# Optimization experiments

Hardware: AMD Instinct MI355X
Metric: run time of the kernel (lower is better)

The kernel has to match this reference:

```python
import jax, jax.numpy as jnp
import numpy as np

IDENTITY_WEIGHT = 0.5
EPS_NORM = 1e-6   # channel RMSNorm eps
EPS_COS = 1e-12   # cosine-sim norm eps (matches torch F.normalize default)


def setup_inputs() -> dict:
    key = jax.random.key(0)
    k1, k2 = jax.random.split(key)
    B, C, H, W = 32, 768, 32, 32
    X = jax.random.normal(k1, (B, C, H, W), dtype=jnp.float32)
    # 1x1 conv weight [out=3C, in=C] (kernel dims squeezed)
    W_in = jax.random.normal(k2, (3 * C, C), dtype=jnp.float32) * (C ** -0.5)
    return {"X": X, "W_in": W_in}


def _cos_sim(t):
    # normalize over the flattened spatial axis (last dim)
    return t / (jnp.linalg.norm(t, axis=-1, keepdims=True) + EPS_COS)


def reference(X, W_in):
    B, C, H, W = X.shape
    # norm: parameter-free RMS over channel dim
    Xn = X * jax.lax.rsqrt(jnp.mean(X * X, axis=1, keepdims=True) + EPS_NORM)
    # 1x1 conv (bias-free) == channel GEMM: [B,3C,H,W]
    qkv = jnp.einsum('oc,bchw->bohw', W_in, Xn)
    K = qkv[:, :C].reshape(B, 1, C, H * W)       # b h c (x y), h=1
    V = qkv[:, C:2 * C].reshape(B, 1, C, H * W)
    # cosine similarity per channel over spatial positions: [B,1,C,1]
    A = jnp.sum(_cos_sim(K) * _cos_sim(V), axis=-1, keepdims=True)
    # affine gate with identity weight (feature_map_attn = identity)
    A = (1.0 - IDENTITY_WEIGHT) * A + IDENTITY_WEIGHT
    A = A.reshape(B, C, 1, 1)  # 'b 1 c 1 -> b c 1 1'
    return A * X
```

## Files before the change

### kernel.cpp

```cpp
#include <hip/hip_runtime.h>
#include <hip/hip_bf16.h>
#include <cstdint>
#include <cstddef>


#define B_   32
#define C_   768
#define HW_  1024
#define CHW_ (C_ * HW_)
#define EPS_NORM 1e-6f
#define EPS_COS  1e-12f

using f32x4  = __attribute__((ext_vector_type(4))) float;
using bf16x8 = __attribute__((ext_vector_type(8))) short;

__device__ inline unsigned short f2bf(float f) {
    union { float f; unsigned u; } v; v.f = f;
    unsigned u = v.u;
    u += 0x7fffu + ((u >> 16) & 1u);
    return (unsigned short)(u >> 16);
}

__device__ __forceinline__ void load16_lds(const unsigned short* g, short* l) {
    __builtin_amdgcn_global_load_lds(
        (const __attribute__((address_space(1))) unsigned int*)g,
        (__attribute__((address_space(3))) unsigned int*)l,
        16, 0, 0);
}

__global__ void wconv_kernel(const float* __restrict__ W, unsigned short* __restrict__ Wbf) {
    const int i = blockIdx.x * 256 + threadIdx.x;
    const float4 v = reinterpret_cast<const float4*>(W)[i];
    ushort4 o;
    o.x = f2bf(v.x); o.y = f2bf(v.y); o.z = f2bf(v.z); o.w = f2bf(v.w);
    reinterpret_cast<ushort4*>(Wbf)[i] = o;
}

__global__ void sumsq_kernel(const float* __restrict__ X, float* __restrict__ ssum) {
    const int b  = blockIdx.y;
    const int c0 = blockIdx.x * 32;
    const int t  = threadIdx.x;
    const float4* xp = reinterpret_cast<const float4*>(X + (size_t)b * CHW_ + (size_t)c0 * HW_) + t;
    float4 s = {0.f, 0.f, 0.f, 0.f};
    #pragma unroll 8
    for (int c = 0; c < 32; ++c) {
        float4 v = xp[c * 256];
        s.x += v.x * v.x; s.y += v.y * v.y; s.z += v.z * v.z; s.w += v.w * v.w;
    }
    float* dst = ssum + b * HW_ + t * 4;
    atomicAdd(dst + 0, s.x);
    atomicAdd(dst + 1, s.y);
    atomicAdd(dst + 2, s.z);
    atomicAdd(dst + 3, s.w);
}

__global__ __launch_bounds__(256) void xnt_kernel(const float* __restrict__ X,
                                                  const float* __restrict__ ssum,
                                                  unsigned short* __restrict__ Xnt) {
    const int b   = blockIdx.z;
    const int c0  = blockIdx.y * 64;
    const int hw0 = blockIdx.x * 64;
    const int tid = threadIdx.x;
    __shared__ short T[64][78];

    #pragma unroll
    for (int it = 0; it < 4; ++it) {
        int q  = it * 256 + tid;
        int r  = q >> 4;
        int c4 = (q & 15) * 4;
        const float4 x = *reinterpret_cast<const float4*>(
            X + (size_t)b * CHW_ + (size_t)(c0 + r) * HW_ + hw0 + c4);
        const float4 s = *reinterpret_cast<const float4*>(ssum + b * HW_ + hw0 + c4);
        ushort4 o;
        o.x = f2bf(x.x * rsqrtf(s.x * (1.f / 768.f) + EPS_NORM));
        o.y = f2bf(x.y * rsqrtf(s.y * (1.f / 768.f) + EPS_NORM));
        o.z = f2bf(x.z * rsqrtf(s.z * (1.f / 768.f) + EPS_NORM));
        o.w = f2bf(x.w * rsqrtf(s.w * (1.f / 768.f) + EPS_NORM));
        *reinterpret_cast<ushort4*>(&T[r][c4]) = o;
    }
    __syncthreads();
    #pragma unroll
    for (int it = 0; it < 2; ++it) {
        int q  = it * 256 + tid;
        int rp = q >> 3;
        int cc = (q & 7) * 8;
        __align__(16) unsigned short tmp[8];
        #pragma unroll
        for (int j = 0; j < 8; ++j) tmp[j] = (unsigned short)T[cc + j][rp];
        *reinterpret_cast<uint4*>(
            Xnt + (size_t)b * CHW_ + (size_t)(hw0 + rp) * C_ + c0 + cc) =
            *reinterpret_cast<const uint4*>(tmp);
    }
}

__global__ __launch_bounds__(256, 2) void gemm_kernel(
        const unsigned short* __restrict__ Wbf,
        const unsigned short* __restrict__ Xnt,
        float* __restrict__ wsA) {
    const int n0   = blockIdx.x * 128;
    const int c0   = blockIdx.y * 128;
    const int b    = blockIdx.z;
    const int tid  = threadIdx.x;
    const int lane = tid & 63;
    const int wave = tid >> 6;
    const int wm   = (wave >> 1) * 64;
    const int wn   = (wave & 1) * 64;
    const int quad = lane >> 4;
    const int l15  = lane & 15;

    __shared__ short sAK[128][64];
    __shared__ short sAV[128][64];
    __shared__ short sB [128][64];

    const f32x4 zero = {0.f, 0.f, 0.f, 0.f};
    f32x4 accK[4][4], accV[4][4];
    #pragma unroll
    for (int i = 0; i < 4; ++i)
        #pragma unroll
        for (int j = 0; j < 4; ++j) { accK[i][j] = zero; accV[i][j] = zero; }

    const size_t wk_base = (size_t)c0 * 768;
    const size_t wv_base = (size_t)(768 + c0) * 768;
    const size_t xb      = (size_t)b * CHW_ + (size_t)n0 * 768;

    size_t goff[4];
    int    lrow[4];
    #pragma unroll
    for (int it = 0; it < 4; ++it) {
        int q   = it * 256 + tid;
        int row = q >> 3;
        int gch = (q & 7) ^ (row & 7);
        goff[it] = (size_t)row * 768 + gch * 8;
        lrow[it] = row & ~7;
    }

    for (int k0 = 0; k0 < 768; k0 += 64) {
        __syncthreads();
        #pragma unroll
        for (int it = 0; it < 4; ++it) {
            load16_lds(Wbf + wk_base + goff[it] + k0, &sAK[lrow[it]][0]);
            load16_lds(Wbf + wv_base + goff[it] + k0, &sAV[lrow[it]][0]);
            load16_lds(Xnt + xb      + goff[it] + k0, &sB [lrow[it]][0]);
        }
        __syncthreads();

        #pragma unroll
        for (int kh = 0; kh < 2; ++kh) {
            bf16x8 aK[4], aV[4], bF[4];
            #pragma unroll
            for (int i = 0; i < 4; ++i) {
                const int rA = wm + 16 * i + l15;
                const int sA = ((kh * 4 + quad) ^ (rA & 7)) * 8;
                aK[i] = *reinterpret_cast<const bf16x8*>(&sAK[rA][sA]);
                aV[i] = *reinterpret_cast<const bf16x8*>(&sAV[rA][sA]);
                const int rB = wn + 16 * i + l15;
                const int sBo = ((kh * 4 + quad) ^ (rB & 7)) * 8;
                bF[i] = *reinterpret_cast<const bf16x8*>(&sB[rB][sBo]);
            }
            #pragma unroll
            for (int i = 0; i < 4; ++i)
                #pragma unroll
                for (int j = 0; j < 4; ++j) {
                    accK[i][j] = __builtin_amdgcn_mfma_f32_16x16x32_bf16(aK[i], bF[j], accK[i][j], 0, 0, 0);
                    accV[i][j] = __builtin_amdgcn_mfma_f32_16x16x32_bf16(aV[i], bF[j], accV[i][j], 0, 0, 0);
                }
        }
    }

    #pragma unroll
    for (int i = 0; i < 4; ++i) {
        #pragma unroll
        for (int r = 0; r < 4; ++r) {
            float pd = 0.f, pk = 0.f, pv = 0.f;
            #pragma unroll
            for (int j = 0; j < 4; ++j) {
                float kk = accK[i][j][r], vv = accV[i][j][r];
                pd += kk * vv; pk += kk * kk; pv += vv * vv;
            }
            #pragma unroll
            for (int off = 1; off < 16; off <<= 1) {
                pd += __shfl_xor(pd, off);
                pk += __shfl_xor(pk, off);
                pv += __shfl_xor(pv, off);
            }
            if (l15 == 0) {
                int c = c0 + wm + 16 * i + 4 * quad + r;
                float* dst = wsA + ((size_t)b * C_ + c) * 3;
                atomicAdd(dst + 0, pd);
                atomicAdd(dst + 1, pk);
                atomicAdd(dst + 2, pv);
            }
        }
    }
}

__global__ void final_kernel(const float* __restrict__ X, const float* __restrict__ wsA,
                             float* __restrict__ out) {
    const int bc = blockIdx.x;
    const float* a = wsA + (size_t)bc * 3;
    const float pd = a[0], pk = a[1], pv = a[2];
    const float A = pd / ((sqrtf(pk) + EPS_COS) * (sqrtf(pv) + EPS_COS));
    const float g = 0.5f * A + 0.5f;
    const size_t i4 = (size_t)bc * 256 + threadIdx.x;
    float4 x = reinterpret_cast<const float4*>(X)[i4];
    float4 o;
    o.x = x.x * g; o.y = x.y * g; o.z = x.z * g; o.w = x.w * g;
    reinterpret_cast<float4*>(out)[i4] = o;
}

extern "C" void kernel_launch(void* const* d_in, const int* in_sizes, int n_in,
                              void* d_out, int out_size, void* d_ws, size_t ws_size,
                              hipStream_t stream) {
    const float* X = (const float*)d_in[0];
    const float* W = (const float*)d_in[1];
    float* out = (float*)d_out;

    char* ws = (char*)d_ws;
    float* wsA           = (float*)ws;
    float* ssum          = (float*)(ws + 294912);
    unsigned short* Wbf  = (unsigned short*)(ws + 425984);
    unsigned short* Xnt  = (unsigned short*)(ws + 2785280);

    hipMemsetAsync(ws, 0, 425984, stream);

    wconv_kernel<<<dim3(1152),       256, 0, stream>>>(W, Wbf);
    sumsq_kernel<<<dim3(24, 32),     256, 0, stream>>>(X, ssum);
    xnt_kernel  <<<dim3(16, 12, 32), 256, 0, stream>>>(X, ssum, Xnt);
    gemm_kernel <<<dim3(8, 6, 32),   256, 0, stream>>>(Wbf, Xnt, wsA);
    final_kernel<<<dim3(24576),      256, 0, stream>>>(X, wsA, out);
}
```

Before: 339.4 us.

## Interleave K/V weight rows and rebuild GEMM as 256x256 ping-pong pipelined kernel

The weight-conversion kernel now interleaves K and V rows so that one A tile holds both, letting each accumulator fragment carry K/V pairs in adjacent lanes. The GEMM grows to 512-thread blocks with 256x256 tiles and double-buffered LDS, where global-to-LDS loads for the next slices are issued while MFMAs run, using explicit waitcnt, barriers and setprio. The aim is to hide memory latency and raise data reuse in the dominant GEMM. In exchange the kernel uses much more LDS and has a fragile hand-written schedule, and the grid has fewer blocks.

```diff
diff --git a/kernel.cpp b/kernel.cpp
--- a/kernel.cpp
+++ b/kernel.cpp
@@ -1,5 +1,4 @@
 #include <hip/hip_runtime.h>
-#include <hip/hip_bf16.h>
 #include <cstdint>
 #include <cstddef>
 
@@ -28,12 +27,20 @@
         16, 0, 0);
 }
 
-__global__ void wconv_kernel(const float* __restrict__ W, unsigned short* __restrict__ Wbf) {
-    const int i = blockIdx.x * 256 + threadIdx.x;
-    const float4 v = reinterpret_cast<const float4*>(W)[i];
+__device__ __forceinline__ void stage_half(const unsigned short* g, short* l,
+                                           size_t toff, int ldsoff, int rs) {
+    load16_lds(g + toff,                     l + ldsoff);
+    load16_lds(g + toff + (size_t)rs * 768,  l + ldsoff + 4096);
+}
+
+__global__ void wconv_kernel(const float* __restrict__ W, unsigned short* __restrict__ Wst) {
+    const int orow = blockIdx.x;
+    const int c4   = threadIdx.x;
+    const int irow = (orow & 1) * 768 + (orow >> 1);
+    const float4 v = reinterpret_cast<const float4*>(W + (size_t)irow * 768)[c4];
     ushort4 o;
     o.x = f2bf(v.x); o.y = f2bf(v.y); o.z = f2bf(v.z); o.w = f2bf(v.w);
-    reinterpret_cast<ushort4*>(Wbf)[i] = o;
+    reinterpret_cast<ushort4*>(Wst + (size_t)orow * 768)[c4] = o;
 }
 
 __global__ void sumsq_kernel(const float* __restrict__ X, float* __restrict__ ssum) {
@@ -93,103 +100,149 @@
     }
 }
 
-__global__ __launch_bounds__(256, 2) void gemm_kernel(
-        const unsigned short* __restrict__ Wbf,
+template<int P, bool VM>
+__device__ __forceinline__ void phase(const short* Ar, const short* Br,
+        const unsigned short* gs, short* ls, size_t toff, int ldsoff, int rs,
+        int l15, int wgm64, int wnl64, int slot0, int slot1,
+        bf16x8 (&bA)[2][2], bf16x8 (&bB)[4][2], f32x4 (&acc)[8][4]) {
+    if constexpr (P == 0) {
+        #pragma unroll
+        for (int ni = 0; ni < 4; ++ni) {
+            const int rB = wnl64 + (ni << 4) + l15;
+            bB[ni][0] = *reinterpret_cast<const bf16x8*>(Br + (rB << 6) + slot0);
+            bB[ni][1] = *reinterpret_cast<const bf16x8*>(Br + (rB << 6) + slot1);
+        }
+    }
+    #pragma unroll
+    for (int s = 0; s < 2; ++s) {
+        const int rA = ((((P & 1) << 1) | s) << 4) + l15 + wgm64;
+        bA[s][0] = *reinterpret_cast<const bf16x8*>(Ar + (rA << 6) + slot0);
+        bA[s][1] = *reinterpret_cast<const bf16x8*>(Ar + (rA << 6) + slot1);
+    }
+    stage_half(gs, ls, toff, ldsoff, rs);
+    if (VM) asm volatile("s_waitcnt vmcnt(6)" ::: "memory");
+    __builtin_amdgcn_sched_barrier(0);
+    __builtin_amdgcn_s_barrier();
+    asm volatile("s_waitcnt lgkmcnt(0)" ::: "memory");
+    __builtin_amdgcn_sched_barrier(0);
+    __builtin_amdgcn_s_setprio(1);
+    #pragma unroll
+    for (int s = 0; s < 2; ++s)
+        #pragma unroll
+        for (int ni = 0; ni < 4; ++ni) {
+            acc[(P << 1) | s][ni] = __builtin_amdgcn_mfma_f32_16x16x32_bf16(
+                bA[s][0], bB[ni][0], acc[(P << 1) | s][ni], 0, 0, 0);
+            acc[(P << 1) | s][ni] = __builtin_amdgcn_mfma_f32_16x16x32_bf16(
+                bA[s][1], bB[ni][1], acc[(P << 1) | s][ni], 0, 0, 0);
+        }
+    __builtin_amdgcn_s_setprio(0);
+    __builtin_amdgcn_sched_barrier(0);
+    __builtin_amdgcn_s_barrier();
+    __builtin_amdgcn_sched_barrier(0);
+}
+
+__global__ __launch_bounds__(512, 2) void gemm_kernel(
+        const unsigned short* __restrict__ Wst,
         const unsigned short* __restrict__ Xnt,
         float* __restrict__ wsA) {
-    const int n0   = blockIdx.x * 128;
-    const int c0   = blockIdx.y * 128;
+    const int n0   = blockIdx.x * 256;
+    const int c0   = blockIdx.y * 256;
     const int b    = blockIdx.z;
     const int tid  = threadIdx.x;
     const int lane = tid & 63;
     const int wave = tid >> 6;
-    const int wm   = (wave >> 1) * 64;
-    const int wn   = (wave & 1) * 64;
+    const int l15  = lane & 15;
     const int quad = lane >> 4;
-    const int l15  = lane & 15;
-
-    __shared__ short sAK[128][64];
-    __shared__ short sAV[128][64];
-    __shared__ short sB [128][64];
-
+    const int wgm64 = (wave >> 2) << 6;
+    const int wq    = wave & 3;
+    const int wnl64 = (wq & 1) << 6;
+    const int hB    = wq >> 1;
+
+    const int lb7   = l15 & 7;
+    const int slot0 = (quad ^ lb7) << 3;
+    const int slot1 = ((quad + 4) ^ lb7) << 3;
+
+    __shared__ __align__(16) short sA[2][2][128][64];
+    __shared__ __align__(16) short sB[2][2][128][64];
+
+    const int r0      = tid >> 3;
+    const size_t toff = (size_t)r0 * 768 + (((tid & 7) ^ (r0 & 7)) << 3);
+    const int ldsoff  = (r0 & ~7) << 6;
+
+    const unsigned short* Ab = Wst + (size_t)c0 * 768;
+    const unsigned short* Bb = Xnt + (size_t)b * CHW_ + (size_t)n0 * 768;
+
+    f32x4 acc[8][4];
     const f32x4 zero = {0.f, 0.f, 0.f, 0.f};
-    f32x4 accK[4][4], accV[4][4];
-    #pragma unroll
-    for (int i = 0; i < 4; ++i)
-        #pragma unroll
-        for (int j = 0; j < 4; ++j) { accK[i][j] = zero; accV[i][j] = zero; }
-
-    const size_t wk_base = (size_t)c0 * 768;
-    const size_t wv_base = (size_t)(768 + c0) * 768;
-    const size_t xb      = (size_t)b * CHW_ + (size_t)n0 * 768;
-
-    size_t goff[4];
-    int    lrow[4];
-    #pragma unroll
-    for (int it = 0; it < 4; ++it) {
-        int q   = it * 256 + tid;
-        int row = q >> 3;
-        int gch = (q & 7) ^ (row & 7);
-        goff[it] = (size_t)row * 768 + gch * 8;
-        lrow[it] = row & ~7;
-    }
-
-    for (int k0 = 0; k0 < 768; k0 += 64) {
-        __syncthreads();
-        #pragma unroll
-        for (int it = 0; it < 4; ++it) {
-            load16_lds(Wbf + wk_base + goff[it] + k0, &sAK[lrow[it]][0]);
-            load16_lds(Wbf + wv_base + goff[it] + k0, &sAV[lrow[it]][0]);
-            load16_lds(Xnt + xb      + goff[it] + k0, &sB [lrow[it]][0]);
-        }
-        __syncthreads();
-
-        #pragma unroll
-        for (int kh = 0; kh < 2; ++kh) {
-            bf16x8 aK[4], aV[4], bF[4];
-            #pragma unroll
-            for (int i = 0; i < 4; ++i) {
-                const int rA = wm + 16 * i + l15;
-                const int sA = ((kh * 4 + quad) ^ (rA & 7)) * 8;
-                aK[i] = *reinterpret_cast<const bf16x8*>(&sAK[rA][sA]);
-                aV[i] = *reinterpret_cast<const bf16x8*>(&sAV[rA][sA]);
-                const int rB = wn + 16 * i + l15;
-                const int sBo = ((kh * 4 + quad) ^ (rB & 7)) * 8;
-                bF[i] = *reinterpret_cast<const bf16x8*>(&sB[rB][sBo]);
-            }
-            #pragma unroll
-            for (int i = 0; i < 4; ++i)
-                #pragma unroll
-                for (int j = 0; j < 4; ++j) {
-                    accK[i][j] = __builtin_amdgcn_mfma_f32_16x16x32_bf16(aK[i], bF[j], accK[i][j], 0, 0, 0);
-                    accV[i][j] = __builtin_amdgcn_mfma_f32_16x16x32_bf16(aV[i], bF[j], accV[i][j], 0, 0, 0);
-                }
-        }
-    }
-
-    #pragma unroll
-    for (int i = 0; i < 4; ++i) {
-        #pragma unroll
-        for (int r = 0; r < 4; ++r) {
-            float pd = 0.f, pk = 0.f, pv = 0.f;
-            #pragma unroll
-            for (int j = 0; j < 4; ++j) {
-                float kk = accK[i][j][r], vv = accV[i][j][r];
-                pd += kk * vv; pk += kk * kk; pv += vv * vv;
-            }
-            #pragma unroll
-            for (int off = 1; off < 16; off <<= 1) {
-                pd += __shfl_xor(pd, off);
-                pk += __shfl_xor(pk, off);
-                pv += __shfl_xor(pv, off);
-            }
-            if (l15 == 0) {
-                int c = c0 + wm + 16 * i + 4 * quad + r;
-                float* dst = wsA + ((size_t)b * C_ + c) * 3;
-                atomicAdd(dst + 0, pd);
-                atomicAdd(dst + 1, pk);
-                atomicAdd(dst + 2, pv);
-            }
+    #pragma unroll
+    for (int i = 0; i < 8; ++i)
+        #pragma unroll
+        for (int j = 0; j < 4; ++j) acc[i][j] = zero;
+
+    bf16x8 bA[2][2], bB[4][2];
+
+    stage_half(Ab,                &sA[0][0][0][0], toff, ldsoff, 128);
+    stage_half(Ab + 64 * 768,     &sA[0][1][0][0], toff, ldsoff, 128);
+    stage_half(Bb,                &sB[0][0][0][0], toff, ldsoff, 64);
+    stage_half(Bb + 128 * 768,    &sB[0][1][0][0], toff, ldsoff, 64);
+    stage_half(Bb + 64,           &sB[1][0][0][0], toff, ldsoff, 64);
+    stage_half(Bb + 128 * 768 + 64, &sB[1][1][0][0], toff, ldsoff, 64);
+    stage_half(Ab + 64,           &sA[1][0][0][0], toff, ldsoff, 128);
+    asm volatile("s_waitcnt vmcnt(6)" ::: "memory");
+    __builtin_amdgcn_s_barrier();
+    __builtin_amdgcn_sched_barrier(0);
+
+    for (int it = 0; it < 6; ++it) {
+        const int kT1 = it * 128 + 64;
+        int kT2 = it * 128 + 128; if (kT2 >= 768) kT2 -= 768;
+        int kT3 = it * 128 + 192; if (kT3 >= 768) kT3 -= 768;
+
+        phase<0, false>(&sA[0][0][0][0], &sB[0][hB][0][0],
+                        Ab + 64 * 768 + kT1, &sA[1][1][0][0], toff, ldsoff, 128,
+                        l15, wgm64, wnl64, slot0, slot1, bA, bB, acc);
+        phase<1, false>(&sA[0][0][0][0], nullptr,
+                        Bb + kT2,            &sB[0][0][0][0], toff, ldsoff, 64,
+                        l15, wgm64, wnl64, slot0, slot1, bA, bB, acc);
+        phase<2, false>(&sA[0][1][0][0], nullptr,
+                        Bb + 128 * 768 + kT2, &sB[0][1][0][0], toff, ldsoff, 64,
+                        l15, wgm64, wnl64, slot0, slot1, bA, bB, acc);
+        phase<3, true >(&sA[0][1][0][0], nullptr,
+                        Ab + kT2,            &sA[0][0][0][0], toff, ldsoff, 128,
+                        l15, wgm64, wnl64, slot0, slot1, bA, bB, acc);
+        phase<0, false>(&sA[1][0][0][0], &sB[1][hB][0][0],
+                        Ab + 64 * 768 + kT2, &sA[0][1][0][0], toff, ldsoff, 128,
+                        l15, wgm64, wnl64, slot0, slot1, bA, bB, acc);
+        phase<1, false>(&sA[1][0][0][0], nullptr,
+                        Bb + kT3,            &sB[1][0][0][0], toff, ldsoff, 64,
+                        l15, wgm64, wnl64, slot0, slot1, bA, bB, acc);
+        phase<2, false>(&sA[1][1][0][0], nullptr,
+                        Bb + 128 * 768 + kT3, &sB[1][1][0][0], toff, ldsoff, 64,
+                        l15, wgm64, wnl64, slot0, slot1, bA, bB, acc);
+        phase<3, true >(&sA[1][1][0][0], nullptr,
+                        Ab + kT3,            &sA[1][0][0][0], toff, ldsoff, 128,
+                        l15, wgm64, wnl64, slot0, slot1, bA, bB, acc);
+    }
+    asm volatile("s_waitcnt vmcnt(0)" ::: "memory");
+
+    #pragma unroll
+    for (int mi = 0; mi < 8; ++mi) {
+        float d0 = 0.f, e0 = 0.f, f0 = 0.f, d1 = 0.f, e1 = 0.f, f1 = 0.f;
+        #pragma unroll
+        for (int ni = 0; ni < 4; ++ni) {
+            f32x4 a = acc[mi][ni];
+            d0 += a[0] * a[1]; e0 += a[0] * a[0]; f0 += a[1] * a[1];
+            d1 += a[2] * a[3]; e1 += a[2] * a[2]; f1 += a[3] * a[3];
+        }
+        #pragma unroll
+        for (int off = 1; off < 16; off <<= 1) {
+            d0 += __shfl_xor(d0, off); e0 += __shfl_xor(e0, off); f0 += __shfl_xor(f0, off);
+            d1 += __shfl_xor(d1, off); e1 += __shfl_xor(e1, off); f1 += __shfl_xor(f1, off);
+        }
+        if (l15 == 0) {
+            const int ch = (c0 >> 1) + wgm64 + (mi << 3) + (quad << 1);
+            float* dst = wsA + ((size_t)b * C_ + ch) * 3;
+            atomicAdd(dst + 0, d0); atomicAdd(dst + 1, e0); atomicAdd(dst + 2, f0);
+            atomicAdd(dst + 3, d1); atomicAdd(dst + 4, e1); atomicAdd(dst + 5, f1);
         }
     }
 }
@@ -218,14 +271,14 @@
     char* ws = (char*)d_ws;
     float* wsA           = (float*)ws;
     float* ssum          = (float*)(ws + 294912);
-    unsigned short* Wbf  = (unsigned short*)(ws + 425984);
+    unsigned short* Wst  = (unsigned short*)(ws + 425984);
     unsigned short* Xnt  = (unsigned short*)(ws + 2785280);
 
     hipMemsetAsync(ws, 0, 425984, stream);
 
-    wconv_kernel<<<dim3(1152),       256, 0, stream>>>(W, Wbf);
+    wconv_kernel<<<dim3(1536),       192, 0, stream>>>(W, Wst);
     sumsq_kernel<<<dim3(24, 32),     256, 0, stream>>>(X, ssum);
     xnt_kernel  <<<dim3(16, 12, 32), 256, 0, stream>>>(X, ssum, Xnt);
-    gemm_kernel <<<dim3(8, 6, 32),   256, 0, stream>>>(Wbf, Xnt, wsA);
+    gemm_kernel <<<dim3(4, 6, 32),   512, 0, stream>>>(Wst, Xnt, wsA);
     final_kernel<<<dim3(24576),      256, 0, stream>>>(X, wsA, out);
 }
```

After: 325.1 us. 4.2% less time.

## Restructure GEMM as persistent B-stationary kernel with interleaved K/V weight streaming

Applied to the files above, without the earlier changes.

Reorders the bf16 weight so each K row is followed by its matching V row. The GEMM becomes a persistent kernel of 256 blocks of 512 threads, each handling two spatial tiles. Each block keeps its activation fragment in registers and streams the weight through double-buffered LDS with explicit vmcnt waits, barriers and a prefetch of the next tile's activations into LDS. The aim is to reuse activations across all 768 channels, cut LDS traffic and overlap loads with MFMA. The cost is heavy register pressure, hand-tuned waitcnt logic that is easy to get wrong, and many more partial atomics per channel.

```diff
diff --git a/kernel.cpp b/kernel.cpp
--- a/kernel.cpp
+++ b/kernel.cpp
@@ -1,5 +1,4 @@
 #include <hip/hip_runtime.h>
-#include <hip/hip_bf16.h>
 #include <cstdint>
 #include <cstddef>
 
@@ -28,12 +27,17 @@
         16, 0, 0);
 }
 
-__global__ void wconv_kernel(const float* __restrict__ W, unsigned short* __restrict__ Wbf) {
-    const int i = blockIdx.x * 256 + threadIdx.x;
-    const float4 v = reinterpret_cast<const float4*>(W)[i];
+#define WAITVM(n) asm volatile("s_waitcnt vmcnt(" #n ")" ::: "memory")
+#define SB0 __builtin_amdgcn_sched_barrier(0)
+
+__global__ void wconv_kernel(const float* __restrict__ W, unsigned short* __restrict__ Wst) {
+    const int orow = blockIdx.x;
+    const int c4   = threadIdx.x;
+    const int irow = (orow & 1) * 768 + (orow >> 1);
+    const float4 v = reinterpret_cast<const float4*>(W + (size_t)irow * 768)[c4];
     ushort4 o;
     o.x = f2bf(v.x); o.y = f2bf(v.y); o.z = f2bf(v.z); o.w = f2bf(v.w);
-    reinterpret_cast<ushort4*>(Wbf)[i] = o;
+    reinterpret_cast<ushort4*>(Wst + (size_t)orow * 768)[c4] = o;
 }
 
 __global__ void sumsq_kernel(const float* __restrict__ X, float* __restrict__ ssum) {
@@ -93,103 +97,143 @@
     }
 }
 
-__global__ __launch_bounds__(256, 2) void gemm_kernel(
-        const unsigned short* __restrict__ Wbf,
+__device__ __forceinline__ void epilogue(f32x4 (&acc)[6], float* wsAb,
+                                         int g48, int m, int quad) {
+    const int chBase = m * 96 + g48 + quad * 2;
+    const f32x4 vz = {0.f, 0.f, 0.f, 0.f};
+    #pragma unroll
+    for (int mi = 0; mi < 6; ++mi) {
+        f32x4 a = acc[mi];
+        float d0 = a[0]*a[1], e0 = a[0]*a[0], f0 = a[1]*a[1];
+        float d1 = a[2]*a[3], e1 = a[2]*a[2], f1 = a[3]*a[3];
+        #pragma unroll
+        for (int off = 1; off < 16; off <<= 1) {
+            d0 += __shfl_xor(d0, off); e0 += __shfl_xor(e0, off); f0 += __shfl_xor(f0, off);
+            d1 += __shfl_xor(d1, off); e1 += __shfl_xor(e1, off); f1 += __shfl_xor(f1, off);
+        }
+        if ((threadIdx.x & 15) == 0) {
+            float* dst = wsAb + (size_t)(chBase + mi * 8) * 3;
+            atomicAdd(dst + 0, d0); atomicAdd(dst + 1, e0); atomicAdd(dst + 2, f0);
+            atomicAdd(dst + 3, d1); atomicAdd(dst + 4, e1); atomicAdd(dst + 5, f1);
+        }
+        acc[mi] = vz;
+    }
+}
+
+template<bool FIRST, bool PREF>
+__device__ __forceinline__ void mstep(
+    const short* Ar0, const short* Ar1, short* st0, short* st1,
+    const unsigned short* gAk, const unsigned short* gAnext,
+    const unsigned short* gBp, short* pB, int prefC,
+    int slot0, int slot1, bf16x8 (&Breg)[24], f32x4 (&acc)[6])
+{
+#define PHASE(kk) do { \
+    if ((kk) == 0)      { if (FIRST) { WAITVM(0); } else { WAITVM(36); } } \
+    else if (PREF && (kk) >= 3 && (kk) <= 6) { WAITVM(1); } \
+    else                { WAITVM(0); } \
+    SB0; __builtin_amdgcn_s_barrier(); SB0; \
+    { short* st_ = ((kk) & 1) ? st0 : st1;                \
+      const unsigned short* g_ = ((kk) < 11) ? (gAk + ((kk) + 1) * 64) : gAnext; \
+      load16_lds(g_,         st_); \
+      load16_lds(g_ + 49152, st_ + 4096); \
+      load16_lds(g_ + 98304, st_ + 8192); } \
+    if (PREF && (kk) >= 2 && (kk) <= 5) \
+      load16_lds(gBp + (size_t)(prefC + (kk) - 2) * 64, pB + (prefC + (kk) - 2) * 4096); \
+    SB0; \
+    { const short* ar_ = ((kk) & 1) ? Ar1 : Ar0;          \
+      __builtin_amdgcn_s_setprio(1); \
+      _Pragma("unroll") \
+      for (int mi_ = 0; mi_ < 6; ++mi_) { \
+        bf16x8 aa0 = *reinterpret_cast<const bf16x8*>(ar_ + (mi_ << 10) + slot0); \
+        bf16x8 aa1 = *reinterpret_cast<const bf16x8*>(ar_ + (mi_ << 10) + slot1); \
+        acc[mi_] = __builtin_amdgcn_mfma_f32_16x16x32_bf16(aa0, Breg[2*(kk)],   acc[mi_], 0, 0, 0); \
+        acc[mi_] = __builtin_amdgcn_mfma_f32_16x16x32_bf16(aa1, Breg[2*(kk)+1], acc[mi_], 0, 0, 0); } \
+      __builtin_amdgcn_s_setprio(0); } \
+    SB0; \
+} while (0)
+    PHASE(0); PHASE(1); PHASE(2); PHASE(3); PHASE(4);  PHASE(5);
+    PHASE(6); PHASE(7); PHASE(8); PHASE(9); PHASE(10); PHASE(11);
+#undef PHASE
+}
+
+__global__ __launch_bounds__(512, 2) void gemm_kernel(
+        const unsigned short* __restrict__ Wst,
         const unsigned short* __restrict__ Xnt,
         float* __restrict__ wsA) {
-    const int n0   = blockIdx.x * 128;
-    const int c0   = blockIdx.y * 128;
-    const int b    = blockIdx.z;
+    const int bid  = blockIdx.x;
     const int tid  = threadIdx.x;
     const int lane = tid & 63;
     const int wave = tid >> 6;
-    const int wm   = (wave >> 1) * 64;
-    const int wn   = (wave & 1) * 64;
+    const int l15  = lane & 15;
     const int quad = lane >> 4;
-    const int l15  = lane & 15;
-
-    __shared__ short sAK[128][64];
-    __shared__ short sAV[128][64];
-    __shared__ short sB [128][64];
-
-    const f32x4 zero = {0.f, 0.f, 0.f, 0.f};
-    f32x4 accK[4][4], accV[4][4];
-    #pragma unroll
-    for (int i = 0; i < 4; ++i)
+    const int lb7  = l15 & 7;
+    const int g96  = (wave >> 2) * 96;
+    const int wn   = (wave & 3) << 4;
+
+    __shared__ __align__(16) short sA[2][192][64];
+    __shared__ __align__(16) short sBpre[96 * 512];
+
+    const int r0      = tid >> 3;
+    const size_t toff = (size_t)r0 * 768 + (((tid & 7) ^ (r0 & 7)) << 3);
+    const int ldsA    = (r0 & ~7) << 6;
+    short* st0 = &sA[0][0][0] + ldsA;
+    short* st1 = &sA[1][0][0] + ldsA;
+    const short* Ar0 = &sA[0][0][0] + ((g96 + l15) << 6);
+    const short* Ar1 = &sA[1][0][0] + ((g96 + l15) << 6);
+    const int slot0 = (quad ^ lb7) << 3;
+    const int slot1 = ((quad + 4) ^ lb7) << 3;
+
+    const int it0 = bid, it1 = bid + 256;
+
+    f32x4 acc[6];
+    const f32x4 vz = {0.f, 0.f, 0.f, 0.f};
+    #pragma unroll
+    for (int i = 0; i < 6; ++i) acc[i] = vz;
+
+    bf16x8 Breg[24];
+    {
+        const unsigned short* gB = Xnt
+            + ((size_t)(it0 >> 4) * HW_ + (size_t)((it0 & 15) << 6) + wn + l15) * 768 + quad * 8;
         #pragma unroll
-        for (int j = 0; j < 4; ++j) { accK[i][j] = zero; accV[i][j] = zero; }
-
-    const size_t wk_base = (size_t)c0 * 768;
-    const size_t wv_base = (size_t)(768 + c0) * 768;
-    const size_t xb      = (size_t)b * CHW_ + (size_t)n0 * 768;
-
-    size_t goff[4];
-    int    lrow[4];
-    #pragma unroll
-    for (int it = 0; it < 4; ++it) {
-        int q   = it * 256 + tid;
-        int row = q >> 3;
-        int gch = (q & 7) ^ (row & 7);
-        goff[it] = (size_t)row * 768 + gch * 8;
-        lrow[it] = row & ~7;
-    }
-
-    for (int k0 = 0; k0 < 768; k0 += 64) {
-        __syncthreads();
-        #pragma unroll
-        for (int it = 0; it < 4; ++it) {
-            load16_lds(Wbf + wk_base + goff[it] + k0, &sAK[lrow[it]][0]);
-            load16_lds(Wbf + wv_base + goff[it] + k0, &sAV[lrow[it]][0]);
-            load16_lds(Xnt + xb      + goff[it] + k0, &sB [lrow[it]][0]);
-        }
-        __syncthreads();
-
-        #pragma unroll
-        for (int kh = 0; kh < 2; ++kh) {
-            bf16x8 aK[4], aV[4], bF[4];
+        for (int ks = 0; ks < 24; ++ks)
+            Breg[ks] = *reinterpret_cast<const bf16x8*>(gB + ks * 32);
+    }
+    const unsigned short* gBp = Xnt
+        + ((size_t)(it1 >> 4) * HW_ + (size_t)((it1 & 15) << 6) + (tid & 63)) * 768
+        + ((tid >> 6) << 3);
+    short* pB = &sBpre[0] + ((tid >> 6) << 9);
+
+    load16_lds(Wst + toff,         st0);
+    load16_lds(Wst + toff + 49152, st0 + 4096);
+    load16_lds(Wst + toff + 98304, st0 + 8192);
+
+    #pragma unroll 1
+    for (int item = 0; item < 2; ++item) {
+        const int itc = (item == 0) ? it0 : it1;
+        float* wsAb = wsA + (size_t)(itc >> 4) * (C_ * 3);
+
+        mstep<true, false>(Ar0, Ar1, st0, st1, Wst + toff, Wst + 147456 + toff,
+                           gBp, pB, 0, slot0, slot1, Breg, acc);
+        epilogue(acc, wsAb, g96 >> 1, 0, quad);
+        #pragma unroll 1
+        for (int m = 1; m < 8; ++m) {
+            const unsigned short* gAk = Wst + (size_t)m * 147456 + toff;
+            const unsigned short* gAn = Wst + (size_t)((m + 1) & 7) * 147456 + toff;
+            if (m >= 2 && m <= 4)
+                mstep<false, true >(Ar0, Ar1, st0, st1, gAk, gAn, gBp, pB, (m - 2) * 4,
+                                    slot0, slot1, Breg, acc);
+            else
+                mstep<false, false>(Ar0, Ar1, st0, st1, gAk, gAn, gBp, pB, 0,
+                                    slot0, slot1, Breg, acc);
+            epilogue(acc, wsAb, g96 >> 1, m, quad);
+        }
+        if (item == 0) {
+            WAITVM(0); SB0;
+            __builtin_amdgcn_s_barrier(); SB0;
             #pragma unroll
-            for (int i = 0; i < 4; ++i) {
-                const int rA = wm + 16 * i + l15;
-                const int sA = ((kh * 4 + quad) ^ (rA & 7)) * 8;
-                aK[i] = *reinterpret_cast<const bf16x8*>(&sAK[rA][sA]);
-                aV[i] = *reinterpret_cast<const bf16x8*>(&sAV[rA][sA]);
-                const int rB = wn + 16 * i + l15;
-                const int sBo = ((kh * 4 + quad) ^ (rB & 7)) * 8;
-                bF[i] = *reinterpret_cast<const bf16x8*>(&sB[rB][sBo]);
-            }
-            #pragma unroll
-            for (int i = 0; i < 4; ++i)
-                #pragma unroll
-                for (int j = 0; j < 4; ++j) {
-                    accK[i][j] = __builtin_amdgcn_mfma_f32_16x16x32_bf16(aK[i], bF[j], accK[i][j], 0, 0, 0);
-                    accV[i][j] = __builtin_amdgcn_mfma_f32_16x16x32_bf16(aV[i], bF[j], accV[i][j], 0, 0, 0);
-                }
-        }
-    }
-
-    #pragma unroll
-    for (int i = 0; i < 4; ++i) {
-        #pragma unroll
-        for (int r = 0; r < 4; ++r) {
-            float pd = 0.f, pk = 0.f, pv = 0.f;
-            #pragma unroll
-            for (int j = 0; j < 4; ++j) {
-                float kk = accK[i][j][r], vv = accV[i][j][r];
-                pd += kk * vv; pk += kk * kk; pv += vv * vv;
-            }
-            #pragma unroll
-            for (int off = 1; off < 16; off <<= 1) {
-                pd += __shfl_xor(pd, off);
-                pk += __shfl_xor(pk, off);
-                pv += __shfl_xor(pv, off);
-            }
-            if (l15 == 0) {
-                int c = c0 + wm + 16 * i + 4 * quad + r;
-                float* dst = wsA + ((size_t)b * C_ + c) * 3;
-                atomicAdd(dst + 0, pd);
-                atomicAdd(dst + 1, pk);
-                atomicAdd(dst + 2, pv);
-            }
+            for (int ks = 0; ks < 24; ++ks)
+                Breg[ks] = *reinterpret_cast<const bf16x8*>(
+                    &sBpre[(ks * 4 + quad) * 512 + ((wn + l15) << 3)]);
         }
     }
 }
@@ -218,14 +262,14 @@
     char* ws = (char*)d_ws;
     float* wsA           = (float*)ws;
     float* ssum          = (float*)(ws + 294912);
-    unsigned short* Wbf  = (unsigned short*)(ws + 425984);
+    unsigned short* Wst  = (unsigned short*)(ws + 425984);
     unsigned short* Xnt  = (unsigned short*)(ws + 2785280);
 
     hipMemsetAsync(ws, 0, 425984, stream);
 
-    wconv_kernel<<<dim3(1152),       256, 0, stream>>>(W, Wbf);
+    wconv_kernel<<<dim3(1536),       192, 0, stream>>>(W, Wst);
     sumsq_kernel<<<dim3(24, 32),     256, 0, stream>>>(X, ssum);
     xnt_kernel  <<<dim3(16, 12, 32), 256, 0, stream>>>(X, ssum, Xnt);
-    gemm_kernel <<<dim3(8, 6, 32),   256, 0, stream>>>(Wbf, Xnt, wsA);
+    gemm_kernel <<<dim3(256),        512, 0, stream>>>(Wst, Xnt, wsA);
     final_kernel<<<dim3(24576),      256, 0, stream>>>(X, wsA, out);
 }
```

After: 674.8 us. 1.99x slower.
